# Kernel optimization log

Hardware: AMD Instinct MI355X
Metric: run time of the kernel (lower is better)

The kernel has to match this reference:

```python
import jax, jax.numpy as jnp
import numpy as np

B, L, H, NL = 32, 1024, 4, 2
D_BERT, D_PHY, D_ACC = 1024, 7, 2
C_IN = D_BERT + D_PHY + D_ACC
D = 32
K = 20
N = B * L
E = N * K


def setup_inputs() -> dict:
    key = jax.random.key(0)
    ks = jax.random.split(key, 10)
    return {
        "protbert": jax.random.normal(ks[0], (B, 1, L, D_BERT), jnp.float32),
        "phychem": jax.random.normal(ks[1], (B, 1, L, D_PHY), jnp.float32),
        "resacc": jax.random.normal(ks[2], (B, 1, L, D_ACC), jnp.float32),
        "edge_feat": jax.random.normal(ks[3], (E, 2), jnp.float32),
        "src_idx": jax.random.randint(ks[4], (E,), 0, N, jnp.int32),
        "dst_idx": (jnp.arange(E, dtype=jnp.int32) % N),  # every node gets exactly K in-edges
        "conv_w": jax.random.normal(ks[5], (D, C_IN, 7), jnp.float32) * 0.02,
        "conv_b": jnp.zeros((D,), jnp.float32),
        "bn_gamma": jnp.ones((D,), jnp.float32),
        "bn_beta": jnp.zeros((D,), jnp.float32),
        "bn_mean": jnp.zeros((D,), jnp.float32),
        "bn_var": jnp.ones((D,), jnp.float32),
        "fc_w": jax.random.normal(ks[6], (NL, H, D, D), jnp.float32) * 0.1,
        "attn_w": jax.random.normal(ks[7], (NL, H, 2 * D + 2), jnp.float32) * 0.1,
        "fc_edge_w": jax.random.normal(ks[8], (NL, H, D, 2), jnp.float32) * 0.1,
        "fc_eatt_w": jax.random.normal(ks[9], (NL, H, 2, 2), jnp.float32) * 0.1,
    }


def _leaky(x):
    return jnp.where(x >= 0, x, 0.01 * x)


def _seg_softmax(e, dst, n):
    # softmax over incoming edges of each destination node (DGL mailbox softmax)
    m = jax.ops.segment_max(e, dst, num_segments=n)
    ex = jnp.exp(e - m[dst])
    s = jax.ops.segment_sum(ex, dst, num_segments=n)
    return ex / s[dst]


def reference(protbert, phychem, resacc, edge_feat, src_idx, dst_idx,
              conv_w, conv_b, bn_gamma, bn_beta, bn_mean, bn_var,
              fc_w, attn_w, fc_edge_w, fc_eatt_w):
    # --- Conv1d + LeakyReLU + BatchNorm1d (eval) encoder ---
    x = jnp.concatenate([protbert, phychem, resacc], axis=3)[:, 0]  # (B,L,C_IN)
    x = jnp.transpose(x, (0, 2, 1))  # (B,C_IN,L)
    x = jax.lax.conv_general_dilated(x, conv_w, (1,), [(3, 3)],
                                     dimension_numbers=("NCH", "OIH", "NCH"))
    x = _leaky(x + conv_b[None, :, None])
    scale = (bn_gamma / jnp.sqrt(bn_var + 1e-5))[None, :, None]
    x = (x - bn_mean[None, :, None]) * scale + bn_beta[None, :, None]
    feats = jnp.transpose(x, (0, 2, 1))  # (B,L,D)

    # --- stacked multi-head EGRET layers on flattened batched graph ---
    h = feats.reshape(N, D)
    alpha = None
    for l in range(NL):
        z = jnp.einsum("nd,hod->nho", h, fc_w[l])                    # (N,H,D)
        ex_t = jnp.einsum("ef,hgf->ehg", edge_feat, fc_eatt_w[l])    # (E,H,2) transformed edge feats for attn
        ez = jnp.einsum("ef,hof->eho", edge_feat, fc_edge_w[l])      # (E,H,D) edge messages
        a_src = attn_w[l][:, :D]
        a_dst = attn_w[l][:, D:2 * D]
        a_e = attn_w[l][:, 2 * D:]
        s_src = jnp.einsum("nhd,hd->nh", z, a_src)                   # node-level partial scores
        s_dst = jnp.einsum("nhd,hd->nh", z, a_dst)
        e = _leaky(s_src[src_idx] + s_dst[dst_idx]
                   + jnp.einsum("ehg,hg->eh", ex_t, a_e))            # (E,H)
        alpha = _seg_softmax(e, dst_idx, N)                          # (E,H)
        msg = alpha[:, :, None] * (z[src_idx] + ez)                  # attn on node+edge messages
        h = jax.ops.segment_sum(msg, dst_idx, num_segments=N).mean(axis=1)  # merge='avg'

    feats2 = h.reshape(B, L, D)
    out = jnp.concatenate([feats2, feats], axis=2)  # (B,L,2D)
    return out, alpha
```

## Files before the change

kernel.cpp:

```cpp
#include <hip/hip_runtime.h>
#include <hip/hip_bf16.h>
#include <cstdint>

#define B_   32
#define L_   1024
#define H_   4
#define NL_  2
#define D_   32
#define K_   20
#define N_   (B_ * L_)
#define E_   (N_ * K_)

typedef __attribute__((ext_vector_type(8))) __bf16 bf16x8;
typedef __attribute__((ext_vector_type(4))) float  f32x4;
typedef __attribute__((ext_vector_type(2))) float  f32x2;
typedef __attribute__((ext_vector_type(4))) int    i32x4;

static __device__ __forceinline__ float leaky1(float x) { return x >= 0.f ? x : 0.01f * x; }

static __device__ __forceinline__ bf16x8 cvt8(f32x4 lo, f32x4 hi) {
    bf16x8 r;
    r[0] = (__bf16)lo[0]; r[1] = (__bf16)lo[1]; r[2] = (__bf16)lo[2]; r[3] = (__bf16)lo[3];
    r[4] = (__bf16)hi[0]; r[5] = (__bf16)hi[1]; r[6] = (__bf16)hi[2]; r[7] = (__bf16)hi[3];
    return r;
}

#define GLD_LDS16(g, l) __builtin_amdgcn_global_load_lds( \
    (const __attribute__((address_space(1))) void*)(g),   \
    (__attribute__((address_space(3))) void*)(l), 16, 0, 0)

__global__ __launch_bounds__(256) void k_prep_wb(const float* __restrict__ conv_w,
                                                 __bf16* __restrict__ wb) {
    int idx = blockIdx.x * 256 + threadIdx.x;
    if (idx >= 7 * 32 * 1024) return;
    int t = idx >> 15;
    int r = idx & 32767;
    int d = r >> 10;
    int c = r & 1023;
    wb[idx] = (__bf16)conv_w[d * 7231 + c * 7 + t];
}

#define XR4 262
__global__ __launch_bounds__(256) void k_conv_part(
    const float* __restrict__ protbert, const __bf16* __restrict__ wb,
    __bf16* __restrict__ pbuf) {
    __shared__ __bf16 Xs[2][XR4 * 32];
    __shared__ __bf16 Bs[2][224 * 32];

    const int tid  = threadIdx.x;
    const int tok0 = blockIdx.x * 256;
    const int b    = tok0 >> 10;
    const int lb   = tok0 & 1023;
    const int cb0  = blockIdx.y * 256;

    const float* agp[5];
    int aoffv[5];
    bool ex[5];
    #pragma unroll
    for (int q = 0; q < 5; ++q) {
        int u = (q < 4) ? q * 256 + tid : 1024 + tid;
        bool e = (q < 4) || (tid < 24);
        int row = u >> 2, slot = u & 3;
        int l = lb + row - 3;
        ex[q] = e;
        aoffv[q] = row * 32 + 8 * (slot ^ ((row >> 1) & 3));
        agp[q] = (e && (unsigned)l < 1024u)
            ? protbert + ((size_t)b * 1024 + l) * 1024 + cb0 + slot * 8 : nullptr;
    }

    const int w     = tid >> 6;
    const int lane  = tid & 63;
    const int row16 = lane & 15;
    const int kgrp  = lane >> 4;
    const int d0    = lane & 15;
    const int bslot0 = 8 * (kgrp ^ ((d0 >> 1) & 3));

    const int blrow = lane >> 2;
    const int bsl   = lane & 3;
#define STAGE_B(kc_, bf_) do {                                              \
        for (int c = w; c < 14; c += 4) {                                   \
            int brow_ = c * 16 + blrow;                                     \
            int dd_ = brow_ & 31;                                           \
            int scol_ = 8 * (bsl ^ ((dd_ >> 1) & 3));                       \
            const __bf16* gp_ = wb + (size_t)brow_ * 1024 + cb0 + (kc_) * 32 + scol_; \
            GLD_LDS16(gp_, &Bs[bf_][c * 512]);                              \
        }                                                                   \
    } while (0)

    f32x4 acc[4][2];
    #pragma unroll
    for (int mt = 0; mt < 4; ++mt) {
        acc[mt][0] = (f32x4){0.f, 0.f, 0.f, 0.f};
        acc[mt][1] = (f32x4){0.f, 0.f, 0.f, 0.f};
    }

    {
        f32x4 pl[5], ph[5];
        #pragma unroll
        for (int q = 0; q < 5; ++q) {
            pl[q] = (f32x4){0,0,0,0}; ph[q] = (f32x4){0,0,0,0};
            if (agp[q]) { pl[q] = ((const f32x4*)agp[q])[0]; ph[q] = ((const f32x4*)agp[q])[1]; }
        }
        STAGE_B(0, 0);
        #pragma unroll
        for (int q = 0; q < 5; ++q)
            if (ex[q]) *(bf16x8*)(&Xs[0][aoffv[q]]) = cvt8(pl[q], ph[q]);
    }
    __syncthreads();

    int buf = 0;
    for (int kk = 0; kk < 8; ++kk) {
        f32x4 nl[5], nh[5];
        if (kk < 7) {
            #pragma unroll
            for (int q = 0; q < 5; ++q) {
                nl[q] = (f32x4){0,0,0,0}; nh[q] = (f32x4){0,0,0,0};
                if (agp[q]) {
                    nl[q] = ((const f32x4*)agp[q])[(kk + 1) * 8];
                    nh[q] = ((const f32x4*)agp[q])[(kk + 1) * 8 + 1];
                }
            }
            STAGE_B(kk + 1, buf ^ 1);
        }
        #pragma unroll
        for (int t = 0; t < 7; ++t) {
            bf16x8 b0 = *(const bf16x8*)(&Bs[buf][(t * 32 + d0) * 32 + bslot0]);
            bf16x8 b1 = *(const bf16x8*)(&Bs[buf][(t * 32 + 16 + d0) * 32 + bslot0]);
            #pragma unroll
            for (int mt = 0; mt < 4; ++mt) {
                int arow = w * 64 + mt * 16 + row16 + t;
                bf16x8 a = *(const bf16x8*)(&Xs[buf][arow * 32 + 8 * (kgrp ^ ((arow >> 1) & 3))]);
                acc[mt][0] = __builtin_amdgcn_mfma_f32_16x16x32_bf16(a, b0, acc[mt][0], 0, 0, 0);
                acc[mt][1] = __builtin_amdgcn_mfma_f32_16x16x32_bf16(a, b1, acc[mt][1], 0, 0, 0);
            }
        }
        if (kk < 7) {
            #pragma unroll
            for (int q = 0; q < 5; ++q)
                if (ex[q]) *(bf16x8*)(&Xs[buf ^ 1][aoffv[q]]) = cvt8(nl[q], nh[q]);
        }
        __syncthreads();
        buf ^= 1;
    }

    __bf16* pb = pbuf + ((size_t)blockIdx.y * N_ + tok0) * 32;
    #pragma unroll
    for (int mt = 0; mt < 4; ++mt)
        #pragma unroll
        for (int i = 0; i < 4; ++i) {
            int lrow = w * 64 + mt * 16 + kgrp * 4 + i;
            pb[lrow * 32 + d0]      = (__bf16)acc[mt][0][i];
            pb[lrow * 32 + 16 + d0] = (__bf16)acc[mt][1][i];
        }
}

#define AROWS 70
__global__ __launch_bounds__(256) void k_epi_z0(
    const __bf16* __restrict__ pbuf,    const float* __restrict__ phychem,
    const float* __restrict__ resacc,   const float* __restrict__ conv_w,
    const float* __restrict__ conv_b,   const float* __restrict__ bn_gamma,
    const float* __restrict__ bn_beta,  const float* __restrict__ bn_mean,
    const float* __restrict__ bn_var,   const float* __restrict__ fc_w,
    const float* __restrict__ attn_w,
    float* __restrict__ out, __bf16* __restrict__ z,
    float* __restrict__ ssrc, float* __restrict__ sdst) {
    __shared__ float WT[4 * 1028];
    __shared__ float As[4 * 33], Ad[4 * 33];
    __shared__ float x9[AROWS * 9];
    __shared__ float w9[9 * 7 * 32];
    __shared__ float bnA[32], bnB[32], cb[32];
    __shared__ float fs[64 * 36];

    const int tid  = threadIdx.x;
    const int tok0 = blockIdx.x * 64;
    const int b    = tok0 >> 10;
    const int lb   = tok0 & 1023;

    for (int i = tid; i < 4096; i += 256) {
        int h = i >> 10, rem = i & 1023, o = rem >> 5, d = rem & 31;
        WT[h * 1028 + d * 32 + o] = fc_w[i];
    }
    {
        int h = tid >> 6, o = tid & 63;
        float v = attn_w[h * 66 + o];
        if (o < 32) As[h * 33 + o] = v; else Ad[h * 33 + (o - 32)] = v;
    }
    for (int i = tid; i < 9 * 7 * 32; i += 256) {
        int d = i & 31, jt = i >> 5, t = jt % 7, j = jt / 7;
        w9[i] = conv_w[d * 7231 + (1024 + j) * 7 + t];
    }
    for (int i = tid; i < AROWS * 9; i += 256) {
        int r = i / 9, j = i % 9;
        int l = lb + r - 3;
        float v = 0.f;
        if ((unsigned)l < 1024u)
            v = (j < 7) ? phychem[(b * 1024 + l) * 7 + j] : resacc[(b * 1024 + l) * 2 + (j - 7)];
        x9[i] = v;
    }
    if (tid < 32) {
        float sc = bn_gamma[tid] * rsqrtf(bn_var[tid] + 1e-5f);
        bnA[tid] = sc;
        bnB[tid] = bn_beta[tid] - bn_mean[tid] * sc;
        cb[tid]  = conv_b[tid];
    }
    __syncthreads();

    {
        const int d  = tid & 31;
        const int r0 = tid >> 5;
        #pragma unroll
        for (int q = 0; q < 8; ++q) {
            int lrow = r0 * 8 + q;
            int tok  = tok0 + lrow;
            float s = (float)pbuf[(size_t)tok * 32 + d]
                    + (float)pbuf[(size_t)(N_ + tok) * 32 + d]
                    + (float)pbuf[(size_t)(2 * N_ + tok) * 32 + d]
                    + (float)pbuf[(size_t)(3 * N_ + tok) * 32 + d];
            float c = 0.f;
            #pragma unroll
            for (int t = 0; t < 7; ++t) {
                const float* xr = &x9[(lrow + t) * 9];
                #pragma unroll
                for (int j = 0; j < 9; ++j) c += xr[j] * w9[(j * 7 + t) * 32 + d];
            }
            float v = leaky1(s + c + cb[d]) * bnA[d] + bnB[d];
            out[(size_t)tok * 64 + 32 + d] = v;
            fs[lrow * 36 + d] = v;
        }
    }
    __syncthreads();

    {
        const int nl = tid >> 2;
        const int h  = tid & 3;
        const int n  = tok0 + nl;

        float hrow[32];
        const f32x4* h4 = (const f32x4*)(&fs[nl * 36]);
        #pragma unroll
        for (int q = 0; q < 8; ++q) {
            f32x4 v = h4[q];
            hrow[q * 4 + 0] = v[0]; hrow[q * 4 + 1] = v[1];
            hrow[q * 4 + 2] = v[2]; hrow[q * 4 + 3] = v[3];
        }
        float zz[32];
        #pragma unroll
        for (int o = 0; o < 32; ++o) zz[o] = 0.f;
        #pragma unroll
        for (int d = 0; d < 32; ++d) {
            float hv = hrow[d];
            const f32x4* wt = (const f32x4*)&WT[h * 1028 + d * 32];
            #pragma unroll
            for (int o4 = 0; o4 < 8; ++o4) {
                f32x4 wv = wt[o4];
                zz[o4 * 4 + 0] += hv * wv[0]; zz[o4 * 4 + 1] += hv * wv[1];
                zz[o4 * 4 + 2] += hv * wv[2]; zz[o4 * 4 + 3] += hv * wv[3];
            }
        }
        float s1 = 0.f, s2 = 0.f;
        #pragma unroll
        for (int o = 0; o < 32; ++o) {
            s1 += zz[o] * As[h * 33 + o];
            s2 += zz[o] * Ad[h * 33 + o];
        }
        bf16x8* zo = (bf16x8*)(z + (size_t)n * 128 + h * 32);
        #pragma unroll
        for (int q = 0; q < 4; ++q) {
            bf16x8 v;
            #pragma unroll
            for (int j = 0; j < 8; ++j) v[j] = (__bf16)zz[q * 8 + j];
            zo[q] = v;
        }
        ssrc[n * 4 + h] = s1;
        sdst[n * 4 + h] = s2;
    }
}

__global__ __launch_bounds__(256) void k_z(
    const float* __restrict__ hin, const float* __restrict__ fc_w,
    const float* __restrict__ attn_w, int layer,
    __bf16* __restrict__ z, float* __restrict__ ssrc, float* __restrict__ sdst) {
    __shared__ float WT[4 * 1028];
    __shared__ float As[4 * 33], Ad[4 * 33];

    const int tid = threadIdx.x;
    for (int i = tid; i < 4096; i += 256) {
        int h = i >> 10, rem = i & 1023, o = rem >> 5, d = rem & 31;
        WT[h * 1028 + d * 32 + o] = fc_w[layer * 4096 + i];
    }
    {
        int h = tid >> 6, o = tid & 63;
        float v = attn_w[layer * (4 * 66) + h * 66 + o];
        if (o < 32) As[h * 33 + o] = v; else Ad[h * 33 + (o - 32)] = v;
    }
    __syncthreads();

    const int n = blockIdx.x * 64 + (tid >> 2);
    const int h = tid & 3;

    float hrow[32];
    const f32x4* h4 = (const f32x4*)(hin + (size_t)n * 32);
    #pragma unroll
    for (int q = 0; q < 8; ++q) {
        f32x4 v = h4[q];
        hrow[q * 4 + 0] = v[0]; hrow[q * 4 + 1] = v[1];
        hrow[q * 4 + 2] = v[2]; hrow[q * 4 + 3] = v[3];
    }

    float zz[32];
    #pragma unroll
    for (int o = 0; o < 32; ++o) zz[o] = 0.f;
    #pragma unroll
    for (int d = 0; d < 32; ++d) {
        float hv = hrow[d];
        const f32x4* wt = (const f32x4*)&WT[h * 1028 + d * 32];
        #pragma unroll
        for (int o4 = 0; o4 < 8; ++o4) {
            f32x4 wv = wt[o4];
            zz[o4 * 4 + 0] += hv * wv[0]; zz[o4 * 4 + 1] += hv * wv[1];
            zz[o4 * 4 + 2] += hv * wv[2]; zz[o4 * 4 + 3] += hv * wv[3];
        }
    }
    float s1 = 0.f, s2 = 0.f;
    #pragma unroll
    for (int o = 0; o < 32; ++o) {
        s1 += zz[o] * As[h * 33 + o];
        s2 += zz[o] * Ad[h * 33 + o];
    }
    bf16x8* zo = (bf16x8*)(z + (size_t)n * 128 + h * 32);
    #pragma unroll
    for (int q = 0; q < 4; ++q) {
        bf16x8 v;
        #pragma unroll
        for (int j = 0; j < 8; ++j) v[j] = (__bf16)zz[q * 8 + j];
        zo[q] = v;
    }
    ssrc[n * 4 + h] = s1;
    sdst[n * 4 + h] = s2;
}

__global__ __launch_bounds__(256) void k_node(
    const __bf16* __restrict__ z, const float* __restrict__ ssrc,
    const float* __restrict__ sdst, const int* __restrict__ src_idx,
    const float* __restrict__ edge_feat, const float* __restrict__ attn_w,
    const float* __restrict__ fc_edge_w, const float* __restrict__ fc_eatt_w,
    int layer, float* __restrict__ hout, int hout_stride,
    float* __restrict__ alpha_out) {
    __shared__ float sWe0[4 * 32], sWe1[4 * 32];
    __shared__ float sP[4][2];
    __shared__ float sAl[4][4][24];
    __shared__ float sF[4][4][2];
    __shared__ float sEf[4][20][2];
    __shared__ int   sS[4][24];

    const int tid = threadIdx.x;
    {
        int f = tid & 1, dd = (tid >> 1) & 31, h = tid >> 6;
        float v = fc_edge_w[layer * 256 + tid];
        if (f == 0) sWe0[h * 32 + dd] = v; else sWe1[h * 32 + dd] = v;
        if (tid < 8) {
            int hh = tid >> 1, ff = tid & 1;
            float ae0 = attn_w[layer * 264 + hh * 66 + 64];
            float ae1 = attn_w[layer * 264 + hh * 66 + 65];
            float w0  = fc_eatt_w[layer * 16 + hh * 4 + 0 + ff];
            float w1  = fc_eatt_w[layer * 16 + hh * 4 + 2 + ff];
            sP[hh][ff] = ae0 * w0 + ae1 * w1;
        }
    }
    const int slot = tid >> 6, tn = tid & 63;
    const int n = blockIdx.x * 4 + slot;
    __syncthreads();

    {
        int h = tn & 3;
        float sdv = sdst[n * 4 + h];
        #pragma unroll
        for (int p = 0; p < 2; ++p) {
            int k = p * 16 + (tn >> 2);
            if (p == 0 || tn < 16) {
                int e = n + k * N_;
                int s = src_idx[e];
                f32x2 ef = *(const f32x2*)(edge_feat + (size_t)e * 2);
                float sc = ssrc[s * 4 + h] + sdv + ef.x * sP[h][0] + ef.y * sP[h][1];
                sAl[slot][h][k] = leaky1(sc);
                if (h == 0) { sS[slot][k] = s; sEf[slot][k][0] = ef.x; sEf[slot][k][1] = ef.y; }
            }
        }
    }
    __syncthreads();

    if (tn < 4) {
        int h = tn;
        float m = -1e30f;
        for (int k = 0; k < 20; ++k) m = fmaxf(m, sAl[slot][h][k]);
        float ssum = 0.f;
        for (int k = 0; k < 20; ++k) {
            float v = __expf(sAl[slot][h][k] - m);
            sAl[slot][h][k] = v;
            ssum += v;
        }
        float inv = 1.f / ssum;
        float F0 = 0.f, F1 = 0.f;
        for (int k = 0; k < 20; ++k) {
            float a = sAl[slot][h][k] * inv;
            sAl[slot][h][k] = a;
            F0 += a * sEf[slot][k][0];
            F1 += a * sEf[slot][k][1];
        }
        sF[slot][h][0] = F0;
        sF[slot][h][1] = F1;
    }
    __syncthreads();

    if (alpha_out != nullptr) {
        #pragma unroll
        for (int p = 0; p < 2; ++p) {
            int k = p * 16 + (tn >> 2), h = tn & 3;
            if (p == 0 || tn < 16)
                alpha_out[(size_t)(n + k * N_) * 4 + h] = sAl[slot][h][k];
        }
    }

    {
        const int h = tn >> 4, dp = tn & 15;
        f32x4 areg[5];
        i32x4 sreg[5];
        #pragma unroll
        for (int q = 0; q < 5; ++q) {
            areg[q] = *(const f32x4*)(&sAl[slot][h][q * 4]);
            sreg[q] = *(const i32x4*)(&sS[slot][q * 4]);
        }
        float F0 = sF[slot][h][0], F1 = sF[slot][h][1];
        float w0a = sWe0[h * 32 + dp * 2], w0b = sWe0[h * 32 + dp * 2 + 1];
        float w1a = sWe1[h * 32 + dp * 2], w1b = sWe1[h * 32 + dp * 2 + 1];
        float acca = F0 * w0a + F1 * w1a;
        float accb = F0 * w0b + F1 * w1b;
        #pragma unroll
        for (int k = 0; k < 20; ++k) {
            int sk = __builtin_amdgcn_readfirstlane(sreg[k >> 2][k & 3]);
            const uint32_t* zp = (const uint32_t*)(z + (size_t)sk * 128);
            uint32_t u = zp[tn];
            float zl = __uint_as_float(u << 16);
            float zh = __uint_as_float(u & 0xffff0000u);
            float a = areg[k >> 2][k & 3];
            acca = fmaf(a, zl, acca);
            accb = fmaf(a, zh, accb);
        }
        acca += __shfl_xor(acca, 16); acca += __shfl_xor(acca, 32);
        accb += __shfl_xor(accb, 16); accb += __shfl_xor(accb, 32);
        if (tn < 16) {
            f32x2 o = {0.25f * acca, 0.25f * accb};
            *(f32x2*)(hout + (size_t)n * hout_stride + dp * 2) = o;
        }
    }
}

extern "C" void kernel_launch(void* const* d_in, const int* in_sizes, int n_in,
                              void* d_out, int out_size, void* d_ws, size_t ws_size,
                              hipStream_t stream) {
    const float* protbert  = (const float*)d_in[0];
    const float* phychem   = (const float*)d_in[1];
    const float* resacc    = (const float*)d_in[2];
    const float* edge_feat = (const float*)d_in[3];
    const int*   src_idx   = (const int*)d_in[4];
    const float* conv_w    = (const float*)d_in[6];
    const float* conv_b    = (const float*)d_in[7];
    const float* bn_gamma  = (const float*)d_in[8];
    const float* bn_beta   = (const float*)d_in[9];
    const float* bn_mean   = (const float*)d_in[10];
    const float* bn_var    = (const float*)d_in[11];
    const float* fc_w      = (const float*)d_in[12];
    const float* attn_w    = (const float*)d_in[13];
    const float* fc_edge_w = (const float*)d_in[14];
    const float* fc_eatt_w = (const float*)d_in[15];

    char* ws = (char*)d_ws;
    __bf16* wb   = (__bf16*)(ws);
    float* h1    = (float*)(ws + (5u  << 20));
    float* ssrc  = (float*)(ws + (9u  << 20));
    float* sdst  = (float*)(ws + (10u << 20));
    __bf16* z    = (__bf16*)(ws + (11u << 20));
    __bf16* pbuf = (__bf16*)(ws + (24u << 20));

    float* out       = (float*)d_out;
    float* alpha_out = out + (size_t)N_ * 64;

    k_prep_wb<<<896, 256, 0, stream>>>(conv_w, wb);
    k_conv_part<<<dim3(128, 4), 256, 0, stream>>>(protbert, wb, pbuf);
    k_epi_z0<<<512, 256, 0, stream>>>(pbuf, phychem, resacc, conv_w, conv_b,
                                      bn_gamma, bn_beta, bn_mean, bn_var,
                                      fc_w, attn_w, out, z, ssrc, sdst);
    k_node<<<N_ / 4, 256, 0, stream>>>(z, ssrc, sdst, src_idx, edge_feat, attn_w,
                                       fc_edge_w, fc_eatt_w, 0, h1, 32, nullptr);
    k_z<<<512, 256, 0, stream>>>(h1, fc_w, attn_w, 1, z, ssrc, sdst);
    k_node<<<N_ / 4, 256, 0, stream>>>(z, ssrc, sdst, src_idx, edge_feat, attn_w,
                                       fc_edge_w, fc_eatt_w, 1, out, 64, alpha_out);
}
```

Measured before the change: 136.1 us.

## Pre-pack conv weights into MFMA fragment layout and load B directly to registers

The prep kernel now writes conv weights in a per-lane MFMA B-fragment order, so each lane reads its fragments with contiguous 16-byte global loads. The LDS staging buffer for B and its LDS reads are removed, and the weights are double-buffered in registers across the k-loop, which is now fully unrolled. This cuts LDS traffic and LDS footprint, which may allow more blocks per CU. In exchange it holds 28 bf16x8 fragments per thread, raising register pressure and the risk of spills or lower occupancy, and every wave in a block re-reads the same weights from global/L2.

```diff
diff --git a/kernel.cpp b/kernel.cpp
--- a/kernel.cpp
+++ b/kernel.cpp
@@ -25,33 +25,42 @@
     return r;
 }
 
-#define GLD_LDS16(g, l) __builtin_amdgcn_global_load_lds( \
-    (const __attribute__((address_space(1))) void*)(g),   \
-    (__attribute__((address_space(3))) void*)(l), 16, 0, 0)
-
-__global__ __launch_bounds__(256) void k_prep_wb(const float* __restrict__ conv_w,
-                                                 __bf16* __restrict__ wb) {
+__global__ __launch_bounds__(256) void k_prep_wbp(const float* __restrict__ conv_w,
+                                                  __bf16* __restrict__ wbp) {
     int idx = blockIdx.x * 256 + threadIdx.x;
-    if (idx >= 7 * 32 * 1024) return;
-    int t = idx >> 15;
-    int r = idx & 32767;
-    int d = r >> 10;
-    int c = r & 1023;
-    wb[idx] = (__bf16)conv_w[d * 7231 + c * 7 + t];
+    if (idx >= 229376) return;
+    int j    = idx & 7;
+    int lane = (idx >> 3) & 63;
+    int half = (idx >> 9) & 1;
+    int cg   = (idx >> 10) & 31;
+    int t    = idx >> 15;
+    int d = half * 16 + (lane & 15);
+    int c = cg * 32 + ((lane >> 4) << 3) + j;
+    wbp[idx] = (__bf16)conv_w[d * 7231 + c * 7 + t];
+}
+
+static __device__ __forceinline__ void load_bfrag(const __bf16* __restrict__ wbp,
+        int cg, int lane, bf16x8 (&br)[7][2]) {
+    #pragma unroll
+    for (int t = 0; t < 7; ++t) {
+        const __bf16* wp = wbp + (size_t)(t * 32 + cg) * 1024 + lane * 8;
+        br[t][0] = *(const bf16x8*)(wp);
+        br[t][1] = *(const bf16x8*)(wp + 512);
+    }
 }
 
 #define XR4 262
 __global__ __launch_bounds__(256) void k_conv_part(
-    const float* __restrict__ protbert, const __bf16* __restrict__ wb,
+    const float* __restrict__ protbert, const __bf16* __restrict__ wbp,
     __bf16* __restrict__ pbuf) {
     __shared__ __bf16 Xs[2][XR4 * 32];
-    __shared__ __bf16 Bs[2][224 * 32];
 
     const int tid  = threadIdx.x;
     const int tok0 = blockIdx.x * 256;
     const int b    = tok0 >> 10;
     const int lb   = tok0 & 1023;
     const int cb0  = blockIdx.y * 256;
+    const int cg0  = blockIdx.y * 8;
 
     const float* agp[5];
     int aoffv[5];
@@ -73,19 +82,6 @@
     const int row16 = lane & 15;
     const int kgrp  = lane >> 4;
     const int d0    = lane & 15;
-    const int bslot0 = 8 * (kgrp ^ ((d0 >> 1) & 3));
-
-    const int blrow = lane >> 2;
-    const int bsl   = lane & 3;
-#define STAGE_B(kc_, bf_) do {                                              \
-        for (int c = w; c < 14; c += 4) {                                   \
-            int brow_ = c * 16 + blrow;                                     \
-            int dd_ = brow_ & 31;                                           \
-            int scol_ = 8 * (bsl ^ ((dd_ >> 1) & 3));                       \
-            const __bf16* gp_ = wb + (size_t)brow_ * 1024 + cb0 + (kc_) * 32 + scol_; \
-            GLD_LDS16(gp_, &Bs[bf_][c * 512]);                              \
-        }                                                                   \
-    } while (0)
 
     f32x4 acc[4][2];
     #pragma unroll
@@ -94,6 +90,8 @@
         acc[mt][1] = (f32x4){0.f, 0.f, 0.f, 0.f};
     }
 
+    bf16x8 brA[7][2], brB[7][2];
+
     {
         f32x4 pl[5], ph[5];
         #pragma unroll
@@ -101,15 +99,18 @@
             pl[q] = (f32x4){0,0,0,0}; ph[q] = (f32x4){0,0,0,0};
             if (agp[q]) { pl[q] = ((const f32x4*)agp[q])[0]; ph[q] = ((const f32x4*)agp[q])[1]; }
         }
-        STAGE_B(0, 0);
+        load_bfrag(wbp, cg0, lane, brA);
         #pragma unroll
         for (int q = 0; q < 5; ++q)
             if (ex[q]) *(bf16x8*)(&Xs[0][aoffv[q]]) = cvt8(pl[q], ph[q]);
     }
     __syncthreads();
 
-    int buf = 0;
+    #pragma unroll
     for (int kk = 0; kk < 8; ++kk) {
+        const int buf = kk & 1;
+        bf16x8 (&brCur)[7][2] = buf ? brB : brA;
+        bf16x8 (&brNxt)[7][2] = buf ? brA : brB;
         f32x4 nl[5], nh[5];
         if (kk < 7) {
             #pragma unroll
@@ -120,12 +121,12 @@
                     nh[q] = ((const f32x4*)agp[q])[(kk + 1) * 8 + 1];
                 }
             }
-            STAGE_B(kk + 1, buf ^ 1);
+            load_bfrag(wbp, cg0 + kk + 1, lane, brNxt);
         }
         #pragma unroll
         for (int t = 0; t < 7; ++t) {
-            bf16x8 b0 = *(const bf16x8*)(&Bs[buf][(t * 32 + d0) * 32 + bslot0]);
-            bf16x8 b1 = *(const bf16x8*)(&Bs[buf][(t * 32 + 16 + d0) * 32 + bslot0]);
+            bf16x8 b0 = brCur[t][0];
+            bf16x8 b1 = brCur[t][1];
             #pragma unroll
             for (int mt = 0; mt < 4; ++mt) {
                 int arow = w * 64 + mt * 16 + row16 + t;
@@ -140,7 +141,6 @@
                 if (ex[q]) *(bf16x8*)(&Xs[buf ^ 1][aoffv[q]]) = cvt8(nl[q], nh[q]);
         }
         __syncthreads();
-        buf ^= 1;
     }
 
     __bf16* pb = pbuf + ((size_t)blockIdx.y * N_ + tok0) * 32;
@@ -475,7 +475,7 @@
     const float* fc_eatt_w = (const float*)d_in[15];
 
     char* ws = (char*)d_ws;
-    __bf16* wb   = (__bf16*)(ws);
+    __bf16* wbp  = (__bf16*)(ws);
     float* h1    = (float*)(ws + (5u  << 20));
     float* ssrc  = (float*)(ws + (9u  << 20));
     float* sdst  = (float*)(ws + (10u << 20));
@@ -485,8 +485,8 @@
     float* out       = (float*)d_out;
     float* alpha_out = out + (size_t)N_ * 64;
 
-    k_prep_wb<<<896, 256, 0, stream>>>(conv_w, wb);
-    k_conv_part<<<dim3(128, 4), 256, 0, stream>>>(protbert, wb, pbuf);
+    k_prep_wbp<<<896, 256, 0, stream>>>(conv_w, wbp);
+    k_conv_part<<<dim3(128, 4), 256, 0, stream>>>(protbert, wbp, pbuf);
     k_epi_z0<<<512, 256, 0, stream>>>(pbuf, phychem, resacc, conv_w, conv_b,
                                       bn_gamma, bn_beta, bn_mean, bn_var,
                                       fc_w, attn_w, out, z, ssrc, sdst);
```

Measured after the change: 135.0 us. Within noise of the previous version (-0.8%).
